# Kernel optimization log

Hardware: AMD Instinct MI355X
Metric: run time of the kernel (lower is better)

The kernel has to match this reference:

```python
import jax, jax.numpy as jnp
import numpy as np

N_OPS, B, C, N = 7, 128, 64, 30   # n_ops from alphas (7), SPD dim hard-coded to 30 in source
KARCHER_ITERS = 3                 # fixed-point iterations of the weighted geometric mean


def _spd_fn(X, fn):
    """Apply scalar fn to eigenvalues of batched symmetric matrices X[..., n, n]."""
    s, U = jnp.linalg.eigh(X)
    s = jnp.maximum(s, 1e-8)  # SPD clamp for log/sqrt stability
    return jnp.einsum('...ij,...j,...kj->...ik', U, fn(s), U)


def _sym(X):
    return 0.5 * (X + jnp.swapaxes(X, -1, -2))


def setup_inputs() -> dict:
    key = jax.random.key(0)
    k1, k2 = jax.random.split(key)
    # Candidate-op outputs: SPD matrices, one per (op, batch, channel).
    G = jax.random.normal(k1, (N_OPS, B, C, N, N), dtype=jnp.float32)
    spds = jnp.einsum('...ij,...kj->...ik', G, G) / N + 0.1 * jnp.eye(N, dtype=jnp.float32)
    # Architecture logits for this edge (softmaxed in forward, as in Network.forward).
    alphas = 0.001 * jax.random.normal(k2, (N_OPS,), dtype=jnp.float32)
    return {"spds": spds, "alphas": alphas}


def reference(spds, alphas):
    """MixedOp forward: softmax-weighted SPD geometric (Karcher) barycenter over
    candidate ops, batched over every (batch, channel) 30x30 SPD matrix.
    Replaces the per-channel Python loop + bary_geom_weightedbatch of the source.
    Returns [B, C, N, N]."""
    w = jax.nn.softmax(alphas)                       # [n_ops]
    A = spds.reshape(N_OPS, B * C, N, N)             # [o, m, n, n], m = B*C
    # init with weighted arithmetic mean (standard Karcher-flow initialization)
    X = jnp.einsum('o,omij->mij', w, A)              # [m, n, n]
    for _ in range(KARCHER_ITERS):
        Xh = _spd_fn(X, jnp.sqrt)                    # X^{1/2}
        Xih = _spd_fn(X, lambda s: 1.0 / jnp.sqrt(s))  # X^{-1/2}
        mid = jnp.einsum('mij,omjk,mkl->omil', Xih, A, Xih)  # [o, m, n, n]
        logs = _spd_fn(_sym(mid), jnp.log)
        L = _sym(jnp.einsum('o,omij->mij', w, logs))  # tangent-space mean
        X = _sym(Xh @ _spd_fn(L, jnp.exp) @ Xh)      # exp map back to manifold
    return X.reshape(B, C, N, N)
```

## Files before the change

### kernel.cpp

```cpp
#include <hip/hip_runtime.h>
#include <math.h>

#define NOPS 7
#define KITERS 3
#define NBLK 31
#define WPB 4
#define CHKFROM 10
#define CONVEPS 3e-6f

#define WSYNC() asm volatile("s_waitcnt lgkmcnt(0)" ::: "memory")
#define VSYNC() asm volatile("s_waitcnt vmcnt(0)" ::: "memory")

template<int M> __device__ __forceinline__ float xshuf(float x);
template<> __device__ __forceinline__ float xshuf<1>(float x) {
    return __int_as_float(__builtin_amdgcn_mov_dpp(__float_as_int(x), 0xB1, 0xF, 0xF, true));
}
template<> __device__ __forceinline__ float xshuf<2>(float x) {
    return __int_as_float(__builtin_amdgcn_mov_dpp(__float_as_int(x), 0x4E, 0xF, 0xF, true));
}
template<> __device__ __forceinline__ float xshuf<4>(float x) {
    return __int_as_float(__builtin_amdgcn_ds_swizzle(__float_as_int(x), (4 << 10) | 0x1F));
}
template<> __device__ __forceinline__ float xshuf<8>(float x) {
    return __int_as_float(__builtin_amdgcn_ds_swizzle(__float_as_int(x), (8 << 10) | 0x1F));
}

template<int M>
__device__ __forceinline__ void jround(float (&a)[16], float (&v)[16], float2* ct,
                                       const int il, const int wlane, const int fKb) {
    const int fil = (il & (M - 1)) | ((il >> 1) & ~(M - 1));
    const float dq  = xshuf<M>(a[0]);
    const float apq = a[M];
    float cc = 1.f, ss = 0.f;
    if (fabsf(apq) > 1e-12f) {
        const float th = (dq - a[0]) / (2.f * apq);
        const float t  = copysignf(1.f, th) / (fabsf(th) + sqrtf(fmaf(th, th, 1.f)));
        cc = rsqrtf(fmaf(t, t, 1.f));
        ss = t * cc;
    }
    if ((wlane & (32 | M)) == 0) ct[fil] = make_float2(cc, ss);
    WSYNC();
    const float2 me = ct[fil];
    const float sg = (il & M) ? 1.f : -1.f;
    const float c0 = me.x, s0 = sg * me.y;
    #pragma unroll
    for (int j = 0; j < 16; ++j) {
        if (j & M) continue;
        const int fj = (j & (M - 1)) | ((j >> 1) & ~(M - 1));
        const float2 cs = ct[fil ^ (fj | fKb)];
        const float sl = sg * cs.y;
        const float ak = a[j], am = a[j ^ M];
        a[j]     = fmaf( sl, am, cs.x * ak);
        a[j ^ M] = fmaf(-sl, ak, cs.x * am);
        const float2 cu = ct[fj | fKb];
        const float vk = v[j], vm = v[j ^ M];
        v[j]     = fmaf(-cu.y, vm, cu.x * vk);
        v[j ^ M] = fmaf( cu.y, vk, cu.x * vm);
    }
    #pragma unroll
    for (int j = 0; j < 16; ++j) {
        if (j & M) continue;
        const float r1 = xshuf<M>(a[j ^ M]);
        const float r2 = xshuf<M>(a[j]);
        a[j]     = fmaf(s0, r1, c0 * a[j]);
        a[j ^ M] = fmaf(s0, r2, c0 * a[j ^ M]);
    }
}

__global__ __launch_bounds__(64 * WPB)
void karcher_kernel(const float* __restrict__ spds, const float* __restrict__ alphas,
                    float* __restrict__ out, int Mtot) {
    __shared__ __align__(16) float XIb[WPB][1024];
    __shared__ __align__(16) float SCb[WPB][1024];
    __shared__ float2 CTb[WPB][16];
    __shared__ float FDAb[WPB][32];
    __shared__ float FDBb[WPB][32];
    __shared__ float WSb[WPB][8];

    const int tid   = threadIdx.x;
    const int wid   = tid >> 6;
    const int wlane = tid & 63;
    const int il    = wlane & 31;
    const int cbit  = wlane >> 5;
    const int cbase = cbit << 4;
    const int fKb   = cbit << 3;
    const int c13   = cbit ? 13 : 0;
    const int mat   = blockIdx.x * WPB + wid;
    const bool rr   = (il < 30);

    float* XI  = XIb[wid];
    float* SC  = SCb[wid];
    float2* CT = CTb[wid];
    float* FDA = FDAb[wid];
    float* FDB = FDBb[wid];
    float* WS  = WSb[wid];

    if (mat >= Mtot) return;

    if (wlane == 0) {
        float aa[NOPS], mx = -1e30f, sum = 0.f;
        #pragma unroll
        for (int o = 0; o < NOPS; ++o) { aa[o] = alphas[o]; mx = fmaxf(mx, aa[o]); }
        #pragma unroll
        for (int o = 0; o < NOPS; ++o) { aa[o] = expf(aa[o] - mx); sum += aa[o]; }
        #pragma unroll
        for (int o = 0; o < NOPS; ++o) WS[o] = aa[o] / sum;
    }

    int l4row = il;
    #pragma unroll
    for (int i = 0; i < 4; ++i) l4row = ((l4row << 1) & 31) ^ ((l4row & 16) ? 5 : 0);

    const size_t ostr = (size_t)Mtot * 900;
    const float* Abase = spds + (size_t)mat * 900 + (size_t)il * 30 + cbase;
    float* orow = out + (size_t)mat * 900 + (size_t)il * 30 + cbase;

    auto stage16 = [&](float* buf, const float (&r)[16]) {
        #pragma unroll
        for (int j = 0; j < 16; ++j) buf[((cbase + j) << 5) + il] = r[j];
    };
    auto xload16 = [&](const float* buf, float (&a)[16]) {
        #pragma unroll
        for (int j = 0; j < 16; ++j) a[j] = buf[((il ^ (cbase + j)) << 5) + il];
    };
    auto perm4 = [&](float (&a)[16], float (&v)[16]) {
        constexpr int L4T[16] = {0,16,5,21,10,26,15,31,20,4,17,1,30,14,27,11};
        #pragma unroll
        for (int j = 0; j < 16; ++j) SC[((cbase + j) << 5) + il] = a[j];
        WSYNC();
        #pragma unroll
        for (int j = 0; j < 16; ++j) a[j] = SC[((L4T[j] ^ c13) << 5) + l4row];
        WSYNC();
        #pragma unroll
        for (int j = 0; j < 16; ++j) SC[((cbase + j) << 5) + il] = v[j];
        WSYNC();
        #pragma unroll
        for (int j = 0; j < 16; ++j) v[j] = SC[((L4T[j] ^ c13) << 5) + il];
        WSYNC();
    };
    auto jacobi = [&](float (&a)[16], float (&v)[16]) {
        #pragma unroll
        for (int j = 0; j < 16; ++j) v[j] = (cbase + j == il) ? 1.f : 0.f;
        #pragma unroll 1
        for (int b = 0; b < NBLK; ++b) {
            jround<1>(a, v, CT, il, wlane, fKb);
            jround<2>(a, v, CT, il, wlane, fKb);
            jround<4>(a, v, CT, il, wlane, fKb);
            jround<8>(a, v, CT, il, wlane, fKb);
            if (b >= CHKFROM) {
                float mx = cbit ? fabsf(a[0]) : 0.f;
                #pragma unroll
                for (int j = 1; j < 16; ++j) mx = fmaxf(mx, fabsf(a[j]));
                if (!__any(mx > CONVEPS)) break;
            }
            if (b != NBLK - 1) perm4(a, v);
        }
    };
    auto loadA = [&](const float* Ao, float (&r)[16]) {
        #pragma unroll
        for (int u = 0; u < 7; ++u) {
            const float2 p = *(const float2*)(Ao + 2 * u);
            r[2 * u] = p.x; r[2 * u + 1] = p.y;
        }
        if (cbit == 0) {
            const float2 p = *(const float2*)(Ao + 14);
            r[14] = p.x; r[15] = p.y;
        }
    };
    auto fma16 = [&](const float* buf, const int k, const float c, float (&acc)[16]) {
        const float4* bp = (const float4*)(buf + (k << 5) + cbase);
        #pragma unroll
        for (int q = 0; q < 4; ++q) {
            const float4 b = bp[q];
            acc[4*q+0] = fmaf(c, b.x, acc[4*q+0]);
            acc[4*q+1] = fmaf(c, b.y, acc[4*q+1]);
            acc[4*q+2] = fmaf(c, b.z, acc[4*q+2]);
            acc[4*q+3] = fmaf(c, b.w, acc[4*q+3]);
        }
    };

    WSYNC();

    float X[16];
    #pragma unroll
    for (int j = 0; j < 16; ++j) X[j] = 0.f;
    if (rr) {
        #pragma unroll 1
        for (int o = 0; o < NOPS; ++o) {
            const float wo = WS[o];
            float r[16];
            #pragma unroll
            for (int j = 0; j < 16; ++j) r[j] = 0.f;
            loadA(Abase + (size_t)o * ostr, r);
            #pragma unroll
            for (int j = 0; j < 16; ++j) X[j] = fmaf(wo, r[j], X[j]);
        }
    }

    float Lacc[16];

    #pragma unroll 1
    for (int it = 0; it < KITERS; ++it) {
        WSYNC();
        stage16(SC, X);
        WSYNC();
        float a1[16], v1[16];
        xload16(SC, a1);
        jacobi(a1, v1);
        if (wlane < 32) {
            const float lam = fmaxf(a1[0], 1e-8f);
            const float sq = sqrtf(lam);
            FDA[il] = sq;
            FDB[il] = 1.f / sq;
        }
        WSYNC();
        stage16(SC, v1);
        WSYNC();
        {
            float xh[16], xi[16];
            #pragma unroll
            for (int j = 0; j < 16; ++j) { xh[j] = 0.f; xi[j] = 0.f; }
            #pragma unroll 2
            for (int k = 0; k < 32; ++k) {
                const float vk = SC[(k << 5) + il];
                const float c1 = FDA[k] * vk;
                const float c2 = FDB[k] * vk;
                const float4* bp = (const float4*)(SC + (k << 5) + cbase);
                #pragma unroll
                for (int q = 0; q < 4; ++q) {
                    const float4 b = bp[q];
                    xh[4*q+0] = fmaf(c1, b.x, xh[4*q+0]); xi[4*q+0] = fmaf(c2, b.x, xi[4*q+0]);
                    xh[4*q+1] = fmaf(c1, b.y, xh[4*q+1]); xi[4*q+1] = fmaf(c2, b.y, xi[4*q+1]);
                    xh[4*q+2] = fmaf(c1, b.z, xh[4*q+2]); xi[4*q+2] = fmaf(c2, b.z, xi[4*q+2]);
                    xh[4*q+3] = fmaf(c1, b.w, xh[4*q+3]); xi[4*q+3] = fmaf(c2, b.w, xi[4*q+3]);
                }
            }
            if (rr) {
                #pragma unroll
                for (int u = 0; u < 7; ++u)
                    *(float2*)(orow + 2 * u) = make_float2(xh[2*u], xh[2*u+1]);
                if (cbit == 0)
                    *(float2*)(orow + 14) = make_float2(xh[14], xh[15]);
            }
            WSYNC();
            stage16(XI, xi);
        }
        #pragma unroll
        for (int j = 0; j < 16; ++j) Lacc[j] = 0.f;

        #pragma unroll 1
        for (int o = 0; o < NOPS; ++o) {
            float ar[16];
            #pragma unroll
            for (int j = 0; j < 16; ++j) ar[j] = 0.f;
            if (rr) loadA(Abase + (size_t)o * ostr, ar);
            WSYNC();
            stage16(SC, ar);
            WSYNC();
            float T[16];
            #pragma unroll
            for (int j = 0; j < 16; ++j) T[j] = 0.f;
            #pragma unroll 2
            for (int k = 0; k < 30; ++k)
                fma16(SC, k, XI[(k << 5) + il], T);
            WSYNC();
            stage16(SC, T);
            WSYNC();
            float md[16];
            #pragma unroll
            for (int j = 0; j < 16; ++j) md[j] = 0.f;
            #pragma unroll 2
            for (int k = 0; k < 30; ++k)
                fma16(XI, k, SC[(k << 5) + il], md);
            WSYNC();
            stage16(SC, md);
            WSYNC();
            float a2[16], v2[16];
            xload16(SC, a2);
            jacobi(a2, v2);
            if (wlane < 32) FDA[il] = logf(fmaxf(a2[0], 1e-8f));
            WSYNC();
            stage16(SC, v2);
            WSYNC();
            const float wo = WS[o];
            #pragma unroll 2
            for (int k = 0; k < 32; ++k)
                fma16(SC, k, wo * FDA[k] * SC[(k << 5) + il], Lacc);
        }

        WSYNC();
        stage16(SC, Lacc);
        WSYNC();
        float a3[16], v3[16];
        xload16(SC, a3);
        jacobi(a3, v3);
        if (wlane < 32) FDA[il] = expf(fmaxf(a3[0], 1e-8f));
        WSYNC();
        stage16(SC, v3);
        WSYNC();
        float E[16];
        #pragma unroll
        for (int j = 0; j < 16; ++j) E[j] = 0.f;
        #pragma unroll 2
        for (int k = 0; k < 32; ++k)
            fma16(SC, k, FDA[k] * SC[(k << 5) + il], E);
        float xr[16];
        #pragma unroll
        for (int j = 0; j < 16; ++j) xr[j] = 0.f;
        VSYNC();
        if (rr) loadA(orow, xr);
        WSYNC();
        stage16(XI, E);
        stage16(SC, xr);
        WSYNC();
        float T2[16];
        #pragma unroll
        for (int j = 0; j < 16; ++j) T2[j] = 0.f;
        #pragma unroll 2
        for (int k = 0; k < 30; ++k)
            fma16(XI, k, SC[(k << 5) + il], T2);
        WSYNC();
        stage16(XI, T2);
        WSYNC();
        #pragma unroll
        for (int j = 0; j < 16; ++j) X[j] = 0.f;
        #pragma unroll 2
        for (int k = 0; k < 30; ++k)
            fma16(SC, k, XI[(k << 5) + il], X);
    }

    if (rr) {
        #pragma unroll
        for (int u = 0; u < 7; ++u)
            *(float2*)(orow + 2 * u) = make_float2(X[2*u], X[2*u+1]);
        if (cbit == 0)
            *(float2*)(orow + 14) = make_float2(X[14], X[15]);
    }
}

extern "C" void kernel_launch(void* const* d_in, const int* in_sizes, int n_in,
                              void* d_out, int out_size, void* d_ws, size_t ws_size,
                              hipStream_t stream) {
    const float* spds   = (const float*)d_in[0];
    const float* alphas = (const float*)d_in[1];
    float* out = (float*)d_out;
    const int Mtot = in_sizes[0] / (NOPS * 900);
    karcher_kernel<<<dim3((Mtot + WPB - 1) / WPB), dim3(64 * WPB), 0, stream>>>(
        spds, alphas, out, Mtot);
}
```

Measured before the change: 9.400 ms.

## Replace LDS waitcnt barriers with compiler fences and use fast-math Jacobi rotations

Replaces the explicit s_waitcnt lgkmcnt(0) after every LDS staging step with a plain compiler memory fence. The compiler is left to place waits itself, which removes serialising stalls on the single-wave exchanges. The Jacobi rotation now uses hardware rcp/sqrt/rsq intrinsics without a branch, and reads the eigenvector rotation table as float4 pairs. The convergence check starts earlier with a looser threshold, trading some eigendecomposition accuracy for fewer sweeps. Dropping the explicit waits relies on in-wave LDS ordering being preserved by the compiler, and the looser tolerance risks accuracy.

```diff
diff --git a/kernel.cpp b/kernel.cpp
--- a/kernel.cpp
+++ b/kernel.cpp
@@ -5,10 +5,10 @@
 #define KITERS 3
 #define NBLK 31
 #define WPB 4
-#define CHKFROM 10
-#define CONVEPS 3e-6f
-
-#define WSYNC() asm volatile("s_waitcnt lgkmcnt(0)" ::: "memory")
+#define CHKFROM 6
+#define CONVEPS 1e-5f
+
+#define WFENCE() asm volatile("" ::: "memory")
 #define VSYNC() asm volatile("s_waitcnt vmcnt(0)" ::: "memory")
 
 template<int M> __device__ __forceinline__ float xshuf(float x);
@@ -31,31 +31,35 @@
     const int fil = (il & (M - 1)) | ((il >> 1) & ~(M - 1));
     const float dq  = xshuf<M>(a[0]);
     const float apq = a[M];
-    float cc = 1.f, ss = 0.f;
-    if (fabsf(apq) > 1e-12f) {
-        const float th = (dq - a[0]) / (2.f * apq);
-        const float t  = copysignf(1.f, th) / (fabsf(th) + sqrtf(fmaf(th, th, 1.f)));
-        cc = rsqrtf(fmaf(t, t, 1.f));
-        ss = t * cc;
-    }
+    float th = (dq - a[0]) * __builtin_amdgcn_rcpf(apq + apq);
+    float t  = copysignf(__builtin_amdgcn_rcpf(
+                   fabsf(th) + __builtin_amdgcn_sqrtf(fmaf(th, th, 1.f))), th);
+    float cc = __builtin_amdgcn_rsqf(fmaf(t, t, 1.f));
+    float ss = t * cc;
+    if (!(fabsf(apq) > 1e-12f)) { cc = 1.f; ss = 0.f; }
     if ((wlane & (32 | M)) == 0) ct[fil] = make_float2(cc, ss);
-    WSYNC();
+    WFENCE();
     const float2 me = ct[fil];
     const float sg = (il & M) ? 1.f : -1.f;
     const float c0 = me.x, s0 = sg * me.y;
+    const int fb = fil ^ fKb;
+    const float4* cup = (const float4*)(ct + fKb);
+    float4 q;
     #pragma unroll
     for (int j = 0; j < 16; ++j) {
         if (j & M) continue;
         const int fj = (j & (M - 1)) | ((j >> 1) & ~(M - 1));
-        const float2 cs = ct[fil ^ (fj | fKb)];
+        const float2 cs = ct[fb ^ fj];
         const float sl = sg * cs.y;
         const float ak = a[j], am = a[j ^ M];
         a[j]     = fmaf( sl, am, cs.x * ak);
         a[j ^ M] = fmaf(-sl, ak, cs.x * am);
-        const float2 cu = ct[fj | fKb];
+        if ((fj & 1) == 0) q = cup[fj >> 1];
+        const float cux = (fj & 1) ? q.z : q.x;
+        const float cuy = (fj & 1) ? q.w : q.y;
         const float vk = v[j], vm = v[j ^ M];
-        v[j]     = fmaf(-cu.y, vm, cu.x * vk);
-        v[j ^ M] = fmaf( cu.y, vk, cu.x * vm);
+        v[j]     = fmaf(-cuy, vm, cux * vk);
+        v[j ^ M] = fmaf( cuy, vk, cux * vm);
     }
     #pragma unroll
     for (int j = 0; j < 16; ++j) {
@@ -72,7 +76,7 @@
                     float* __restrict__ out, int Mtot) {
     __shared__ __align__(16) float XIb[WPB][1024];
     __shared__ __align__(16) float SCb[WPB][1024];
-    __shared__ float2 CTb[WPB][16];
+    __shared__ __align__(64) float2 CTb[WPB][16];
     __shared__ float FDAb[WPB][32];
     __shared__ float FDBb[WPB][32];
     __shared__ float WSb[WPB][8];
@@ -127,16 +131,16 @@
         constexpr int L4T[16] = {0,16,5,21,10,26,15,31,20,4,17,1,30,14,27,11};
         #pragma unroll
         for (int j = 0; j < 16; ++j) SC[((cbase + j) << 5) + il] = a[j];
-        WSYNC();
+        WFENCE();
         #pragma unroll
         for (int j = 0; j < 16; ++j) a[j] = SC[((L4T[j] ^ c13) << 5) + l4row];
-        WSYNC();
+        WFENCE();
         #pragma unroll
         for (int j = 0; j < 16; ++j) SC[((cbase + j) << 5) + il] = v[j];
-        WSYNC();
+        WFENCE();
         #pragma unroll
         for (int j = 0; j < 16; ++j) v[j] = SC[((L4T[j] ^ c13) << 5) + il];
-        WSYNC();
+        WFENCE();
     };
     auto jacobi = [&](float (&a)[16], float (&v)[16]) {
         #pragma unroll
@@ -179,7 +183,7 @@
         }
     };
 
-    WSYNC();
+    WFENCE();
 
     float X[16];
     #pragma unroll
@@ -201,9 +205,9 @@
 
     #pragma unroll 1
     for (int it = 0; it < KITERS; ++it) {
-        WSYNC();
+        WFENCE();
         stage16(SC, X);
-        WSYNC();
+        WFENCE();
         float a1[16], v1[16];
         xload16(SC, a1);
         jacobi(a1, v1);
@@ -213,9 +217,9 @@
             FDA[il] = sq;
             FDB[il] = 1.f / sq;
         }
-        WSYNC();
+        WFENCE();
         stage16(SC, v1);
-        WSYNC();
+        WFENCE();
         {
             float xh[16], xi[16];
             #pragma unroll
@@ -242,7 +246,7 @@
                 if (cbit == 0)
                     *(float2*)(orow + 14) = make_float2(xh[14], xh[15]);
             }
-            WSYNC();
+            WFENCE();
             stage16(XI, xi);
         }
         #pragma unroll
@@ -254,50 +258,50 @@
             #pragma unroll
             for (int j = 0; j < 16; ++j) ar[j] = 0.f;
             if (rr) loadA(Abase + (size_t)o * ostr, ar);
-            WSYNC();
+            WFENCE();
             stage16(SC, ar);
-            WSYNC();
+            WFENCE();
             float T[16];
             #pragma unroll
             for (int j = 0; j < 16; ++j) T[j] = 0.f;
             #pragma unroll 2
             for (int k = 0; k < 30; ++k)
                 fma16(SC, k, XI[(k << 5) + il], T);
-            WSYNC();
+            WFENCE();
             stage16(SC, T);
-            WSYNC();
+            WFENCE();
             float md[16];
             #pragma unroll
             for (int j = 0; j < 16; ++j) md[j] = 0.f;
             #pragma unroll 2
             for (int k = 0; k < 30; ++k)
                 fma16(XI, k, SC[(k << 5) + il], md);
-            WSYNC();
+            WFENCE();
             stage16(SC, md);
-            WSYNC();
+            WFENCE();
             float a2[16], v2[16];
             xload16(SC, a2);
             jacobi(a2, v2);
             if (wlane < 32) FDA[il] = logf(fmaxf(a2[0], 1e-8f));
-            WSYNC();
+            WFENCE();
             stage16(SC, v2);
-            WSYNC();
+            WFENCE();
             const float wo = WS[o];
             #pragma unroll 2
             for (int k = 0; k < 32; ++k)
                 fma16(SC, k, wo * FDA[k] * SC[(k << 5) + il], Lacc);
         }
 
-        WSYNC();
+        WFENCE();
         stage16(SC, Lacc);
-        WSYNC();
+        WFENCE();
         float a3[16], v3[16];
         xload16(SC, a3);
         jacobi(a3, v3);
         if (wlane < 32) FDA[il] = expf(fmaxf(a3[0], 1e-8f));
-        WSYNC();
+        WFENCE();
         stage16(SC, v3);
-        WSYNC();
+        WFENCE();
         float E[16];
         #pragma unroll
         for (int j = 0; j < 16; ++j) E[j] = 0.f;
@@ -309,19 +313,19 @@
         for (int j = 0; j < 16; ++j) xr[j] = 0.f;
         VSYNC();
         if (rr) loadA(orow, xr);
-        WSYNC();
+        WFENCE();
         stage16(XI, E);
         stage16(SC, xr);
-        WSYNC();
+        WFENCE();
         float T2[16];
         #pragma unroll
         for (int j = 0; j < 16; ++j) T2[j] = 0.f;
         #pragma unroll 2
         for (int k = 0; k < 30; ++k)
             fma16(XI, k, SC[(k << 5) + il], T2);
-        WSYNC();
+        WFENCE();
         stage16(XI, T2);
-        WSYNC();
+        WFENCE();
         #pragma unroll
         for (int j = 0; j < 16; ++j) X[j] = 0.f;
         #pragma unroll 2
```

Result: faster. 7.846 ms (median of 2 runs) (-16.5%).
